# Performance work log

Hardware: AMD Instinct MI355X
Metric: run time of the kernel (lower is better)

The kernel has to match this reference:

```python
import jax, jax.numpy as jnp
import numpy as np

NUM_EXPERTS = 8
IN_FEATURES = 2048
OUT_FEATURES = 2048
TOTAL_TOKENS = 32768


def setup_inputs() -> dict:
    key = jax.random.key(0)
    k1, k2, k3 = jax.random.split(key, 3)
    input_tokens = jax.random.normal(k1, (TOTAL_TOKENS, IN_FEATURES), dtype=jnp.float32)
    expert_assignments = jax.random.randint(k2, (TOTAL_TOKENS,), 0, NUM_EXPERTS, dtype=jnp.int32)
    # kaiming_uniform_ with a=sqrt(2): bound = sqrt(6 / ((1 + a^2) * fan_in)) = sqrt(2 / fan_in)
    bound = float(np.sqrt(2.0 / IN_FEATURES))
    weight = jax.random.uniform(k3, (NUM_EXPERTS, OUT_FEATURES, IN_FEATURES),
                                dtype=jnp.float32, minval=-bound, maxval=bound)
    return {"input_tokens": input_tokens, "expert_assignments": expert_assignments, "weight": weight}


def reference(input_tokens, expert_assignments, weight):
    # Grouped GEMM: out[t] = input_tokens[t] @ weight[assign[t]].T
    # Each token belongs to exactly one expert, so masked accumulation over the
    # small fixed expert set reproduces the original sort+per-expert-mm+scatter math.
    num_experts = weight.shape[0]
    out = jnp.zeros((input_tokens.shape[0], weight.shape[1]), dtype=input_tokens.dtype)
    for e in range(num_experts):
        mask = (expert_assignments == e)[:, None]  # [T, 1]
        # zero out tokens not owned by this expert before the GEMM so the
        # contribution is exact (matmul of zero rows yields zero rows)
        xe = jnp.where(mask, input_tokens, 0.0)  # [T, in]
        out = out + xe @ weight[e].T  # [T, out]
    return out
```

## Files before the change

### kernel.cpp

```cpp
#include <hip/hip_runtime.h>
#include <hip/hip_bf16.h>

#define NEXP 8
#define KIN 2048
#define NOUT 2048
#define NTOK 32768

#define BM 256
#define BN 256
#define BK 64

#define NBLK (NTOK / 256)
#define MAXTILE (NTOK / BM + NEXP - 1)

typedef unsigned int u32;
typedef unsigned short u16;
typedef __bf16 bf16x8 __attribute__((ext_vector_type(8)));
typedef float f32x4 __attribute__((ext_vector_type(4)));

__device__ __forceinline__ u16 f2bf(float f) {
    u32 u = __float_as_uint(f);
    u += 0x7FFFu + ((u >> 16) & 1u);
    return (u16)(u >> 16);
}

__device__ __forceinline__ void load_lds16(const void* g, void* l) {
    __builtin_amdgcn_global_load_lds(
        (const __attribute__((address_space(1))) u32*)g,
        (__attribute__((address_space(3))) u32*)l, 16, 0, 0);
}

__global__ void rank_k(const int* __restrict__ assign, int* __restrict__ counts,
                       int* __restrict__ rank, int* __restrict__ blockBase) {
    __shared__ int lc[NEXP];
    int t = blockIdx.x * 256 + threadIdx.x;
    if (threadIdx.x < NEXP) lc[threadIdx.x] = 0;
    __syncthreads();
    int e = assign[t];
    rank[t] = atomicAdd(&lc[e], 1);
    __syncthreads();
    if (threadIdx.x < NEXP)
        blockBase[blockIdx.x * NEXP + threadIdx.x] =
            atomicAdd(&counts[threadIdx.x], lc[threadIdx.x]);
}

__global__ void prefix_k(int* __restrict__ ctrl, int4* __restrict__ tileTable) {
    if (threadIdx.x == 0) {
        int ts = 0, tile = 0;
        for (int e = 0; e < NEXP; e++) {
            ctrl[8 + e] = ts;
            int c = ctrl[e];
            int ntile = (c + BM - 1) / BM;
            for (int i = 0; i < ntile; i++)
                tileTable[tile++] = make_int4(ts + i * BM, ts + c, e, 0);
            ts += c;
        }
        ctrl[8 + NEXP] = ts;
        for (; tile < MAXTILE; tile++) tileTable[tile] = make_int4(0, 0, 0, 0);
    }
}

__global__ void scatter_k(const int* __restrict__ assign, const int* __restrict__ ctrl,
                          const int* __restrict__ rank, const int* __restrict__ blockBase,
                          int* __restrict__ list) {
    __shared__ int base[NEXP];
    int t = blockIdx.x * 256 + threadIdx.x;
    if (threadIdx.x < NEXP)
        base[threadIdx.x] = ctrl[8 + threadIdx.x] +
                            blockBase[blockIdx.x * NEXP + threadIdx.x];
    __syncthreads();
    list[base[assign[t]] + rank[t]] = t;
}

__global__ void conv_k(const float* __restrict__ src, u16* __restrict__ dst) {
    size_t i = ((size_t)blockIdx.x * 256 + threadIdx.x) << 3;
    const float4* s = (const float4*)(src + i);
    float4 f0 = s[0], f1 = s[1];
    uint4 o;
    o.x = (u32)f2bf(f0.x) | ((u32)f2bf(f0.y) << 16);
    o.y = (u32)f2bf(f0.z) | ((u32)f2bf(f0.w) << 16);
    o.z = (u32)f2bf(f1.x) | ((u32)f2bf(f1.y) << 16);
    o.w = (u32)f2bf(f1.z) | ((u32)f2bf(f1.w) << 16);
    *(uint4*)(dst + i) = o;
}

#define BARS() asm volatile("s_barrier" ::: "memory")
#define WVM(N) asm volatile("s_waitcnt vmcnt(" #N ")" ::: "memory")

__global__ __launch_bounds__(512, 2) void gemm_k(const u16* __restrict__ Ab,
                                                 const u16* __restrict__ Wb,
                                                 const int* __restrict__ list,
                                                 const int4* __restrict__ tileTable,
                                                 float* __restrict__ out) {
    extern __shared__ char sh[];
    int* listLds = (int*)(sh + 131072);

    int4 tt = tileTable[blockIdx.y];
    int rowBase = tt.x, rowEnd = tt.y, e = tt.z;
    if (rowEnd <= rowBase) return;
    int nBase = blockIdx.x * BN;
    int tid = threadIdx.x;
    int lane = tid & 63, w = tid >> 6;
    int wm = w >> 2, wn = w & 3;

    if (tid < BM) listLds[tid] = list[min(rowBase + tid, rowEnd - 1)];
    __syncthreads();

    int srow = (w << 4) + (lane >> 3);
    u32 ksoB = (u32)((((lane & 7) ^ (lane >> 3)) << 4));
    u32 aO00 = (u32)listLds[srow] * 4096u + ksoB;
    u32 aO01 = (u32)listLds[srow + 8] * 4096u + ksoB;
    u32 aO10 = (u32)listLds[srow + 128] * 4096u + ksoB;
    u32 aO11 = (u32)listLds[srow + 136] * 4096u + ksoB;
    u32 bO0 = (u32)(e * NOUT + nBase + srow) * 4096u + ksoB;
    u32 bO1 = bO0 + 128u * 4096u;
    u32 ldsOff = (u32)((w << 11) + (lane << 4));

#define STA(H, m, b) { char* d_ = sh + (b) * 65536 + (H) * 16384 + ldsOff;          \
        load_lds16((const char*)Ab + aO##H##0 + (m) * 128, d_);                      \
        load_lds16((const char*)Ab + aO##H##1 + (m) * 128, d_ + 1024); }
#define STB(H, m, b) { char* d_ = sh + (b) * 65536 + 32768 + (H) * 16384 + ldsOff;   \
        load_lds16((const char*)Wb + bO##H + (m) * 128, d_);                         \
        load_lds16((const char*)Wb + bO##H + 32768u + (m) * 128, d_ + 1024); }

    u32 s0 = (u32)((((lane >> 4) ^ (lane & 7)) << 4));
    u32 aRow = (u32)((wm * 128 + (lane & 15)) * 128);
    u32 bRow = (u32)(32768 + (wn * 64 + (lane & 15)) * 128);

    bf16x8 ra0[4][2], ra1[4][2], rb0[2][2], rb1[2][2];
    f32x4 acc[8][4];
#pragma unroll
    for (int i = 0; i < 8; ++i)
#pragma unroll
        for (int j = 0; j < 4; ++j) acc[i][j] = (f32x4){0.f, 0.f, 0.f, 0.f};

#define RDA(dst, mf0, b) { _Pragma("unroll") for (int m_ = 0; m_ < 4; ++m_) {        \
        const char* p_ = sh + (b) * 65536 + aRow + ((mf0) + m_) * 2048;              \
        dst[m_][0] = *(const bf16x8*)(p_ + s0);                                      \
        dst[m_][1] = *(const bf16x8*)(p_ + (s0 ^ 64)); } }
#define RDB(dst, nf0, b) { _Pragma("unroll") for (int n_ = 0; n_ < 2; ++n_) {        \
        const char* p_ = sh + (b) * 65536 + bRow + ((nf0) + n_) * 2048;              \
        dst[n_][0] = *(const bf16x8*)(p_ + s0);                                      \
        dst[n_][1] = *(const bf16x8*)(p_ + (s0 ^ 64)); } }

#define QUAD(RA, RB, MO, NO) { __builtin_amdgcn_s_setprio(1);                        \
    _Pragma("unroll") for (int m_ = 0; m_ < 4; ++m_)                                 \
    _Pragma("unroll") for (int n_ = 0; n_ < 2; ++n_) {                               \
        acc[(MO)+m_][(NO)+n_] = __builtin_amdgcn_mfma_f32_16x16x32_bf16(             \
            RA[m_][0], RB[n_][0], acc[(MO)+m_][(NO)+n_], 0, 0, 0);                   \
        acc[(MO)+m_][(NO)+n_] = __builtin_amdgcn_mfma_f32_16x16x32_bf16(             \
            RA[m_][1], RB[n_][1], acc[(MO)+m_][(NO)+n_], 0, 0, 0); }                 \
    __builtin_amdgcn_s_setprio(0); }

    STA(0, 0, 0); STA(1, 0, 0); STB(0, 0, 0); STB(1, 0, 0);
    STB(0, 1, 1); STB(1, 1, 1); STA(0, 1, 1);
    WVM(6);
    BARS();
    RDA(ra0, 0, 0); RDB(rb0, 0, 0);

    for (int j = 0; j < 30; ++j) {
        int b = j & 1, nb = b ^ 1;
        RDB(rb1, 2, b);
        STA(1, j + 1, nb);
        QUAD(ra0, rb0, 0, 0);
        BARS();
        RDA(ra1, 4, b);
        STB(0, j + 2, b);
        QUAD(ra0, rb1, 0, 2);
        BARS();
        STB(1, j + 2, b);
        QUAD(ra1, rb0, 4, 0);
        BARS();
        WVM(4);
        BARS();
        RDA(ra0, 0, nb);
        RDB(rb0, 0, nb);
        STA(0, j + 2, b);
        QUAD(ra1, rb1, 4, 2);
        BARS();
    }

    RDB(rb1, 2, 0);
    STA(1, 31, 1);
    QUAD(ra0, rb0, 0, 0);
    BARS();
    RDA(ra1, 4, 0);
    QUAD(ra0, rb1, 0, 2);
    BARS();
    QUAD(ra1, rb0, 4, 0);
    BARS();
    WVM(0);
    BARS();
    RDA(ra0, 0, 1);
    RDB(rb0, 0, 1);
    QUAD(ra1, rb1, 4, 2);
    RDB(rb1, 2, 1);
    QUAD(ra0, rb0, 0, 0);
    RDA(ra1, 4, 1);
    QUAD(ra0, rb1, 0, 2);
    QUAD(ra1, rb0, 4, 0);
    QUAD(ra1, rb1, 4, 2);

    int cnt = rowEnd - rowBase;
    int cb = nBase + wn * 64 + (lane & 15);
#pragma unroll
    for (int mf = 0; mf < 8; ++mf) {
        int r0 = wm * 128 + mf * 16 + ((lane >> 4) << 2);
#pragma unroll
        for (int rr = 0; rr < 4; ++rr) {
            int rl = r0 + rr;
            if (rl < cnt) {
                float* orow = out + (size_t)listLds[rl] * NOUT + cb;
#pragma unroll
                for (int nf = 0; nf < 4; ++nf) orow[nf * 16] = acc[mf][nf][rr];
            }
        }
    }
#undef STA
#undef STB
#undef RDA
#undef RDB
#undef QUAD
}

__global__ void fallback_k(const float* __restrict__ A, const int* __restrict__ assign,
                           const float* __restrict__ W, float* __restrict__ out) {
    long idx = (long)blockIdx.x * 256 + threadIdx.x;
    int t = (int)(idx >> 11);
    int n = (int)(idx & (NOUT - 1));
    int e = assign[t];
    const float4* a = (const float4*)(A + (size_t)t * KIN);
    const float4* w = (const float4*)(W + ((size_t)e * NOUT + n) * KIN);
    float s = 0.f;
    for (int k = 0; k < KIN / 4; k++) {
        float4 x = a[k], y = w[k];
        s += x.x * y.x + x.y * y.y + x.z * y.z + x.w * y.w;
    }
    out[idx] = s;
}

extern "C" void kernel_launch(void* const* d_in, const int* in_sizes, int n_in,
                              void* d_out, int out_size, void* d_ws, size_t ws_size,
                              hipStream_t stream) {
    const float* A = (const float*)d_in[0];
    const int* assign = (const int*)d_in[1];
    const float* W = (const float*)d_in[2];
    float* out = (float*)d_out;

    const size_t Ab_bytes = (size_t)NTOK * KIN * 2;
    const size_t Wb_bytes = (size_t)NEXP * NOUT * KIN * 2;
    const size_t list_bytes = (size_t)NTOK * 4;
    const size_t rank_bytes = (size_t)NTOK * 4;
    const size_t bb_bytes = (size_t)NBLK * NEXP * 4;
    const size_t ctrl_bytes = 256;
    const size_t tt_bytes = (size_t)MAXTILE * 16;
    const size_t need = Ab_bytes + Wb_bytes + list_bytes + rank_bytes +
                        bb_bytes + ctrl_bytes + tt_bytes;

    if (ws_size < need) {
        fallback_k<<<(NTOK * (long)NOUT) / 256, 256, 0, stream>>>(A, assign, W, out);
        return;
    }

    char* p = (char*)d_ws;
    u16* Ab = (u16*)p;                     p += Ab_bytes;
    u16* Wb = (u16*)p;                     p += Wb_bytes;
    int* list = (int*)p;                   p += list_bytes;
    int* rank = (int*)p;                   p += rank_bytes;
    int* blockBase = (int*)p;              p += bb_bytes;
    int* ctrl = (int*)p;                   p += ctrl_bytes;
    int4* tileTable = (int4*)p;

    static bool attr_done = false;
    if (!attr_done) {
        hipFuncSetAttribute((const void*)gemm_k,
                            hipFuncAttributeMaxDynamicSharedMemorySize, 132096);
        attr_done = true;
    }

    hipMemsetAsync(ctrl, 0, ctrl_bytes, stream);
    rank_k<<<NBLK, 256, 0, stream>>>(assign, ctrl, rank, blockBase);
    prefix_k<<<1, 64, 0, stream>>>(ctrl, tileTable);
    scatter_k<<<NBLK, 256, 0, stream>>>(assign, ctrl, rank, blockBase, list);
    conv_k<<<(NTOK * (KIN / 8)) / 256, 256, 0, stream>>>(A, Ab);
    conv_k<<<(NEXP * NOUT * (KIN / 8)) / 256, 256, 0, stream>>>(W, Wb);
    dim3 grid(NOUT / BN, MAXTILE);
    gemm_k<<<grid, 512, 132096, stream>>>(Ab, Wb, list, tileTable, out);
}
```

Before: 804.4 us.

## Parallelize tile table build, fuse conversions, remap GEMM grid for XCD locality

The tile table in prefix_k is now built by many threads rather than a single thread, and the two fp32-to-bf16 conversion launches are merged into one kernel. The GEMM grid becomes 1D and its block index is remapped so that consecutive blocks sharing an XCD (orig & 7) handle the same expert tile across N columns. The goals are fewer launches and less serial work, plus better L2 reuse of A rows within each XCD. The remap assumes round-robin placement of blocks across 8 XCDs.

```diff
diff --git a/kernel.cpp b/kernel.cpp
--- a/kernel.cpp
+++ b/kernel.cpp
@@ -45,18 +45,30 @@
 }
 
 __global__ void prefix_k(int* __restrict__ ctrl, int4* __restrict__ tileTable) {
-    if (threadIdx.x == 0) {
-        int ts = 0, tile = 0;
+    __shared__ int cnt[NEXP], ts[NEXP + 1], tstart[NEXP + 1];
+    int t = threadIdx.x;
+    if (t < NEXP) cnt[t] = ctrl[t];
+    __syncthreads();
+    if (t == 0) {
+        int s = 0, tile = 0;
         for (int e = 0; e < NEXP; e++) {
-            ctrl[8 + e] = ts;
-            int c = ctrl[e];
-            int ntile = (c + BM - 1) / BM;
-            for (int i = 0; i < ntile; i++)
-                tileTable[tile++] = make_int4(ts + i * BM, ts + c, e, 0);
-            ts += c;
+            ts[e] = s; tstart[e] = tile;
+            s += cnt[e]; tile += (cnt[e] + BM - 1) / BM;
         }
-        ctrl[8 + NEXP] = ts;
-        for (; tile < MAXTILE; tile++) tileTable[tile] = make_int4(0, 0, 0, 0);
+        ts[NEXP] = s; tstart[NEXP] = tile;
+        for (int e = 0; e <= NEXP; e++) ctrl[8 + e] = ts[e];
+    }
+    __syncthreads();
+    for (int tt = t; tt < MAXTILE; tt += blockDim.x) {
+        int4 v = make_int4(0, 0, 0, 0);
+#pragma unroll
+        for (int e = 0; e < NEXP; e++) {
+            if (tt >= tstart[e] && tt < tstart[e + 1]) {
+                int i = tt - tstart[e];
+                v = make_int4(ts[e] + i * BM, ts[e] + cnt[e], e, 0);
+            }
+        }
+        tileTable[tt] = v;
     }
 }
 
@@ -72,8 +84,13 @@
     list[base[assign[t]] + rank[t]] = t;
 }
 
-__global__ void conv_k(const float* __restrict__ src, u16* __restrict__ dst) {
-    size_t i = ((size_t)blockIdx.x * 256 + threadIdx.x) << 3;
+__global__ void conv2_k(const float* __restrict__ A, u16* __restrict__ Ab,
+                        const float* __restrict__ W, u16* __restrict__ Wb) {
+    const size_t AV = (size_t)NTOK * KIN / 8;
+    size_t v = (size_t)blockIdx.x * 256 + threadIdx.x;
+    const float* src; u16* dst; size_t i;
+    if (v < AV) { src = A; dst = Ab; i = v << 3; }
+    else        { src = W; dst = Wb; i = (v - AV) << 3; }
     const float4* s = (const float4*)(src + i);
     float4 f0 = s[0], f1 = s[1];
     uint4 o;
@@ -95,10 +112,12 @@
     extern __shared__ char sh[];
     int* listLds = (int*)(sh + 131072);
 
-    int4 tt = tileTable[blockIdx.y];
+    int orig = blockIdx.x;
+    int sid = (orig & 7) * (MAXTILE) + (orig >> 3);
+    int4 tt = tileTable[sid >> 3];
     int rowBase = tt.x, rowEnd = tt.y, e = tt.z;
     if (rowEnd <= rowBase) return;
-    int nBase = blockIdx.x * BN;
+    int nBase = (sid & 7) * BN;
     int tid = threadIdx.x;
     int lane = tid & 63, w = tid >> 6;
     int wm = w >> 2, wn = w & 3;
@@ -280,10 +299,9 @@
 
     hipMemsetAsync(ctrl, 0, ctrl_bytes, stream);
     rank_k<<<NBLK, 256, 0, stream>>>(assign, ctrl, rank, blockBase);
-    prefix_k<<<1, 64, 0, stream>>>(ctrl, tileTable);
+    prefix_k<<<1, 256, 0, stream>>>(ctrl, tileTable);
     scatter_k<<<NBLK, 256, 0, stream>>>(assign, ctrl, rank, blockBase, list);
-    conv_k<<<(NTOK * (KIN / 8)) / 256, 256, 0, stream>>>(A, Ab);
-    conv_k<<<(NEXP * NOUT * (KIN / 8)) / 256, 256, 0, stream>>>(W, Wb);
-    dim3 grid(NOUT / BN, MAXTILE);
-    gemm_k<<<grid, 512, 132096, stream>>>(Ab, Wb, list, tileTable, out);
-}
+    const int conv_blocks = (int)(((size_t)NTOK * KIN / 8 + (size_t)NEXP * NOUT * KIN / 8) / 256);
+    conv2_k<<<conv_blocks, 256, 0, stream>>>(A, Ab, W, Wb);
+    gemm_k<<<8 * MAXTILE, 512, 132096, stream>>>(Ab, Wb, list, tileTable, out);
+}
```

Measured after the change: 789.3 us. No clear change (-1.9%).
